# Kernel optimization log

Hardware: AMD Instinct MI355X
Metric: run time of the kernel (lower is better)

Reference implementation:

```python
import jax, jax.numpy as jnp
import numpy as np
import math

B, L, D, H = 4, 2048, 1024, 16
DK = D // H


def setup_inputs() -> dict:
    key = jax.random.key(0)
    ks = jax.random.split(key, 12)
    scale = math.sqrt(6.0 / (D + D))  # xavier_uniform for square Linear
    def lin(k):
        return jax.random.uniform(k, (D, D), jnp.float32, -scale, scale)
    inp = {
        "query": jax.random.normal(ks[0], (B, L, D), jnp.float32),
        "key": jax.random.normal(ks[1], (B, L, D), jnp.float32),
        "value": jax.random.normal(ks[2], (B, L, D), jnp.float32),
        "Wq": lin(ks[3]), "bq": jnp.zeros((D,), jnp.float32),
        "Wk": lin(ks[4]), "bk": jnp.zeros((D,), jnp.float32),
        "Wv": lin(ks[5]), "bv": jnp.zeros((D,), jnp.float32),
        "Wo": lin(ks[6]), "bo": jnp.zeros((D,), jnp.float32),
        # causal mask: True means masked (hide future positions)
        "attn_mask": jnp.triu(jnp.ones((L, L), dtype=bool), k=1),
    }
    return inp


def reference(query, key, value, Wq, bq, Wk, bk, Wv, bv, Wo, bo, attn_mask):
    def proj(x, W, b):
        # torch Linear: x @ W.T + b ; then split heads -> [B, H, L, DK]
        y = jnp.einsum('bld,ed->ble', x, W) + b
        return y.reshape(B, L, H, DK).transpose(0, 2, 1, 3)

    q = proj(query, Wq, bq)
    k = proj(key, Wk, bk)
    v = proj(value, Wv, bv)

    scores = jnp.einsum('bhqd,bhkd->bhqk', q, k) / jnp.sqrt(jnp.float32(DK))
    scores = jnp.where(attn_mask[None, None, :, :], jnp.float32(-jnp.inf), scores)
    p_attn = jax.nn.softmax(scores, axis=-1)  # dropout p=0 (eval)

    ctx = jnp.einsum('bhqk,bhkd->bhqd', p_attn, v)
    ctx = ctx.transpose(0, 2, 1, 3).reshape(B, L, D)
    out = jnp.einsum('bld,ed->ble', ctx, Wo) + bo
    return out
```

## Files before the change

### kernel.cpp

```cpp
#include <hip/hip_runtime.h>
#include <hip/hip_bf16.h>
#include <stdint.h>

typedef unsigned short u16;
typedef unsigned int u32;
typedef short short8 __attribute__((ext_vector_type(8)));
typedef float f32x4 __attribute__((ext_vector_type(4)));
typedef u32 u32x4 __attribute__((ext_vector_type(4)));
typedef u32 u32x2 __attribute__((ext_vector_type(2)));

#define DEV static __device__ __forceinline__

constexpr int Bsz = 4, Lseq = 2048, Dm = 1024, Hn = 16, Dk = 64;
constexpr float LOG2E = 1.44269504088896340736f;
constexpr float QSCALE = 0.125f * LOG2E;

DEV u16 f2bf(float x) {
    u32 u = __builtin_bit_cast(u32, x);
    return (u16)((u + 0x7fffu + ((u >> 16) & 1u)) >> 16);
}

DEV u32 pk2(float a, float b) {
    __hip_bfloat162 h = __float22bfloat162_rn(float2{a, b});
    u32 r;
    __builtin_memcpy(&r, &h, 4);
    return r;
}

DEV u32x4 ld8_cvt(const float* p) {
    f32x4 lo = *(const f32x4*)p;
    f32x4 hi = *(const f32x4*)(p + 4);
    u32x4 r;
    r[0] = pk2(lo[0], lo[1]);
    r[1] = pk2(lo[2], lo[3]);
    r[2] = pk2(hi[0], hi[1]);
    r[3] = pk2(hi[2], hi[3]);
    return r;
}

DEV void glds16(const void* g, void* l) {
    __builtin_amdgcn_global_load_lds(
        (const __attribute__((address_space(1))) void*)g,
        (__attribute__((address_space(3))) void*)l, 16, 0, 0);
}

__global__ __launch_bounds__(256) void cvt_f2b(
    const float* __restrict__ s, u16* __restrict__ d, int n8)
{
    int i = blockIdx.x * 256 + threadIdx.x;
    if (i >= n8) return;
    ((u32x4*)d)[i] = ld8_cvt(s + (long)i * 8);
}

template <int MODE>
__global__ __launch_bounds__(256) void gemm_glds(
    const u16* __restrict__ A, const u16* __restrict__ Bw,
    const float* __restrict__ bias, void* __restrict__ Cout, float scale)
{
    __shared__ u16 At[2][128 * 32];
    __shared__ u16 Bt[2][128 * 32];

    const int tid = threadIdx.x;
    const int lane = tid & 63, wid = tid >> 6;
    const int wr = wid >> 1, wc = wid & 1;
    const int mbase = blockIdx.x * 128, nbase = blockIdx.y * 128;

    f32x4 acc[4][4];
#pragma unroll
    for (int i = 0; i < 4; i++)
#pragma unroll
        for (int j = 0; j < 4; j++) acc[i][j] = (f32x4)0.f;

    const int srow = lane >> 2;
    const int sseg = (lane & 3) * 8;

    auto stage = [&](int kt, int buf) {
#pragma unroll
        for (int c = 0; c < 2; c++) {
            const int sec = wid * 2 + c;
            const long ko = (long)kt * 32 + sseg;
            glds16(A + (long)(mbase + sec * 16 + srow) * Dm + ko, &At[buf][sec * 512]);
            glds16(Bw + (long)(nbase + sec * 16 + srow) * Dm + ko, &Bt[buf][sec * 512]);
        }
    };

    stage(0, 0);
    __syncthreads();

    for (int kt = 0; kt < 32; kt++) {
        const int cur = kt & 1;
        if (kt + 1 < 32) stage(kt + 1, cur ^ 1);
        short8 af[4], bfr[4];
#pragma unroll
        for (int mf = 0; mf < 4; mf++)
            af[mf] = *(const short8*)&At[cur][(wr * 64 + mf * 16 + (lane & 15)) * 32 + (lane >> 4) * 8];
#pragma unroll
        for (int nf = 0; nf < 4; nf++)
            bfr[nf] = *(const short8*)&Bt[cur][(wc * 64 + nf * 16 + (lane & 15)) * 32 + (lane >> 4) * 8];
        __builtin_amdgcn_s_setprio(1);
#pragma unroll
        for (int mf = 0; mf < 4; mf++)
#pragma unroll
            for (int nf = 0; nf < 4; nf++)
                acc[mf][nf] = __builtin_amdgcn_mfma_f32_16x16x32_bf16(af[mf], bfr[nf], acc[mf][nf], 0, 0, 0);
        __builtin_amdgcn_s_setprio(0);
        __syncthreads();
    }

#pragma unroll
    for (int nf = 0; nf < 4; nf++) {
        const int n = nbase + wc * 64 + nf * 16 + (lane & 15);
        const float bv = bias[n];
#pragma unroll
        for (int mf = 0; mf < 4; mf++) {
            const int m0 = mbase + wr * 64 + mf * 16 + (lane >> 4) * 4;
#pragma unroll
            for (int r = 0; r < 4; r++) {
                const int m = m0 + r;
                const float v = (acc[mf][nf][r] + bv) * scale;
                if (MODE == 0) {
                    int b = m >> 11, l = m & 2047, h = n >> 6, dk = n & 63;
                    long addr = ((long)(b * Hn + h) * Lseq + l) * Dk + dk;
                    ((u16*)Cout)[addr] = f2bf(v);
                } else {
                    ((float*)Cout)[(long)m * Dm + n] = v;
                }
            }
        }
    }
}

__global__ __launch_bounds__(256) void gemm_hyb(
    const float* __restrict__ X, const u16* __restrict__ Bw,
    const float* __restrict__ bias, u16* __restrict__ Cout, float scale)
{
    __shared__ u16 At[2][128 * 32];
    __shared__ u16 Bt[2][128 * 32];

    const int tid = threadIdx.x;
    const int lane = tid & 63, wid = tid >> 6;
    const int wr = wid >> 1, wc = wid & 1;
    const int mbase = blockIdx.x * 128, nbase = blockIdx.y * 128;

    f32x4 acc[4][4];
#pragma unroll
    for (int i = 0; i < 4; i++)
#pragma unroll
        for (int j = 0; j < 4; j++) acc[i][j] = (f32x4)0.f;

    const int srow = lane >> 2;
    const int sseg = (lane & 3) * 8;
    auto stageB = [&](int kt, int buf) {
#pragma unroll
        for (int c = 0; c < 2; c++) {
            const int sec = wid * 2 + c;
            glds16(Bw + (long)(nbase + sec * 16 + srow) * Dm + (long)kt * 32 + sseg,
                   &Bt[buf][sec * 512]);
        }
    };

    u32x4 va[2];
    auto loadA = [&](int kt) {
#pragma unroll
        for (int i = 0; i < 2; i++) {
            int idx = i * 256 + tid;
            int row = idx >> 2, seg = idx & 3;
            va[i] = ld8_cvt(X + (long)(mbase + row) * Dm + (long)kt * 32 + seg * 8);
        }
    };
    auto writeA = [&](int buf) {
#pragma unroll
        for (int i = 0; i < 2; i++) {
            int idx = i * 256 + tid;
            *(u32x4*)&At[buf][idx * 8] = va[i];
        }
    };

    stageB(0, 0);
    loadA(0);
    writeA(0);
    __syncthreads();

    for (int kt = 0; kt < 32; kt++) {
        const int cur = kt & 1;
        const bool more = (kt + 1 < 32);
        if (more) {
            stageB(kt + 1, cur ^ 1);
            loadA(kt + 1);
        }
        short8 af[4], bfr[4];
#pragma unroll
        for (int mf = 0; mf < 4; mf++)
            af[mf] = *(const short8*)&At[cur][(wr * 64 + mf * 16 + (lane & 15)) * 32 + (lane >> 4) * 8];
#pragma unroll
        for (int nf = 0; nf < 4; nf++)
            bfr[nf] = *(const short8*)&Bt[cur][(wc * 64 + nf * 16 + (lane & 15)) * 32 + (lane >> 4) * 8];
        __builtin_amdgcn_s_setprio(1);
#pragma unroll
        for (int mf = 0; mf < 4; mf++)
#pragma unroll
            for (int nf = 0; nf < 4; nf++)
                acc[mf][nf] = __builtin_amdgcn_mfma_f32_16x16x32_bf16(af[mf], bfr[nf], acc[mf][nf], 0, 0, 0);
        __builtin_amdgcn_s_setprio(0);
        if (more) writeA(cur ^ 1);
        __syncthreads();
    }

#pragma unroll
    for (int nf = 0; nf < 4; nf++) {
        const int n = nbase + wc * 64 + nf * 16 + (lane & 15);
        const float bv = bias[n];
#pragma unroll
        for (int mf = 0; mf < 4; mf++) {
            const int m0 = mbase + wr * 64 + mf * 16 + (lane >> 4) * 4;
#pragma unroll
            for (int r = 0; r < 4; r++) {
                const int m = m0 + r;
                const float v = (acc[mf][nf][r] + bv) * scale;
                int b = m >> 11, l = m & 2047, h = n >> 6, dk = n & 63;
                long addr = ((long)(b * Hn + h) * Lseq + l) * Dk + dk;
                Cout[addr] = f2bf(v);
            }
        }
    }
}

__global__ __launch_bounds__(256) void attn_fwd(
    const u16* __restrict__ Qb, const u16* __restrict__ Kb,
    const u16* __restrict__ Vb, u16* __restrict__ Ctx)
{
    __shared__ u16 Kt[2][64 * 64];
    __shared__ u16 Vt[2][64 * 64];
    __shared__ u16 Pq[4][32 * 64];

    const int tid = threadIdx.x, lane = tid & 63, w = tid >> 6;
    const int qt = gridDim.y - 1 - blockIdx.y;
    const int bh = blockIdx.x;
    const long base = (long)bh * Lseq * Dk;
    const int qw = qt * 128 + w * 32;

    const int krow_in_w = lane >> 3;
    const int kseg = lane & 7;
    const int skv = tid >> 3, sdb = (tid & 7) * 8;

    auto stage_k = [&](int kvbase, int buf) {
#pragma unroll
        for (int c = 0; c < 2; c++) {
            int kv = w * 16 + c * 8 + krow_in_w;
            int d0 = ((kseg ^ (kv & 7)) * 8);
            glds16(Kb + base + (long)(kvbase + kv) * Dk + d0,
                   &Kt[buf][(w * 16 + c * 8) * 64]);
        }
    };

    short8 qfr[2][2];
#pragma unroll
    for (int qf = 0; qf < 2; qf++)
#pragma unroll
        for (int ks = 0; ks < 2; ks++) {
            int q = qw + qf * 16 + (lane & 15);
            int d0 = ks * 32 + (lane >> 4) * 8;
            qfr[qf][ks] = *(const short8*)(Qb + base + (long)q * Dk + d0);
        }

    f32x4 accT[4][2];
#pragma unroll
    for (int i = 0; i < 4; i++)
#pragma unroll
        for (int j = 0; j < 2; j++) accT[i][j] = (f32x4)0.f;
    float m_run[2] = {-__builtin_inff(), -__builtin_inff()};
    float l_part[2] = {0.f, 0.f};

    u32x4 vr[2];
    stage_k(0, 0);
#pragma unroll
    for (int i = 0; i < 2; i++)
        vr[i] = *(const u32x4*)(Vb + base + (long)(i * 32 + skv) * Dk + sdb);
#pragma unroll
    for (int i = 0; i < 2; i++) {
        int kv = i * 32 + skv;
        const u16* pv = (const u16*)&vr[i];
#pragma unroll
        for (int j = 0; j < 8; j++) {
            int d = sdb + j;
            Vt[0][d * 64 + (kv ^ ((((d & 7) ^ (d >> 3)) & 7) << 3))] = pv[j];
        }
    }
    __syncthreads();

    const int nkv = qt * 2 + 2;
    const int myn = ((qw + 31) >> 6) + 1;

    for (int kvt = 0; kvt < nkv; kvt++) {
        const int cur = kvt & 1;
        const bool more = (kvt + 1 < nkv);
        const int kvbase = kvt * 64;

        if (more) {
            stage_k(kvbase + 64, cur ^ 1);
#pragma unroll
            for (int i = 0; i < 2; i++)
                vr[i] = *(const u32x4*)(Vb + base + (long)(kvbase + 64 + i * 32 + skv) * Dk + sdb);
        }

        if (kvt < myn) {
            f32x4 st[4][2];
#pragma unroll
            for (int i = 0; i < 4; i++)
#pragma unroll
                for (int j = 0; j < 2; j++) st[i][j] = (f32x4)0.f;
            __builtin_amdgcn_s_setprio(1);
#pragma unroll
            for (int ks = 0; ks < 2; ks++) {
                short8 kf[4];
#pragma unroll
                for (int kvf = 0; kvf < 4; kvf++) {
                    int row = kvf * 16 + (lane & 15);
                    int d0 = ks * 32 + (lane >> 4) * 8;
                    kf[kvf] = *(const short8*)&Kt[cur][row * 64 + (d0 ^ ((row & 7) << 3))];
                }
#pragma unroll
                for (int kvf = 0; kvf < 4; kvf++)
#pragma unroll
                    for (int qf = 0; qf < 2; qf++)
                        st[kvf][qf] = __builtin_amdgcn_mfma_f32_16x16x32_bf16(kf[kvf], qfr[qf][ks], st[kvf][qf], 0, 0, 0);
            }
            __builtin_amdgcn_s_setprio(0);

            if ((kvbase + 63) > qw) {
#pragma unroll
                for (int qf = 0; qf < 2; qf++) {
                    const int q = qw + qf * 16 + (lane & 15);
#pragma unroll
                    for (int kvf = 0; kvf < 4; kvf++)
#pragma unroll
                        for (int r = 0; r < 4; r++) {
                            int kv = kvbase + kvf * 16 + (lane >> 4) * 4 + r;
                            if (kv > q) st[kvf][qf][r] = -1e30f;
                        }
                }
            }

#pragma unroll
            for (int qf = 0; qf < 2; qf++) {
                float tmax = st[0][qf][0];
#pragma unroll
                for (int kvf = 0; kvf < 4; kvf++)
#pragma unroll
                    for (int r = 0; r < 4; r++) tmax = fmaxf(tmax, st[kvf][qf][r]);
                tmax = fmaxf(tmax, __shfl_xor(tmax, 16, 64));
                tmax = fmaxf(tmax, __shfl_xor(tmax, 32, 64));
                const bool norescale = __all((int)(tmax <= m_run[qf] + 8.f));
                if (!norescale) {
                    const float mnew = fmaxf(m_run[qf], tmax);
                    const float sc = __builtin_exp2f(m_run[qf] - mnew);
                    m_run[qf] = mnew;
                    l_part[qf] *= sc;
#pragma unroll
                    for (int dkf = 0; dkf < 4; dkf++)
#pragma unroll
                        for (int r = 0; r < 4; r++) accT[dkf][qf][r] *= sc;
                }
                const float mq = m_run[qf];
                float ts = 0.f;
#pragma unroll
                for (int kvf = 0; kvf < 4; kvf++)
#pragma unroll
                    for (int r = 0; r < 4; r++) {
                        float p = __builtin_exp2f(st[kvf][qf][r] - mq);
                        st[kvf][qf][r] = p;
                        ts += p;
                    }
                l_part[qf] += ts;
                const int qrow = qf * 16 + (lane & 15);
#pragma unroll
                for (int kvf = 0; kvf < 4; kvf++) {
                    u32x2 pk;
                    pk[0] = pk2(st[kvf][qf][0], st[kvf][qf][1]);
                    pk[1] = pk2(st[kvf][qf][2], st[kvf][qf][3]);
                    int kvi = (kvf * 16 + (lane >> 4) * 4) ^ ((lane & 7) << 3);
                    *(u32x2*)&Pq[w][qrow * 64 + kvi] = pk;
                }
            }

#pragma unroll
            for (int kf2 = 0; kf2 < 2; kf2++) {
                short8 vfr[4];
#pragma unroll
                for (int dkf = 0; dkf < 4; dkf++) {
                    int d = dkf * 16 + (lane & 15);
                    int kvi = (kf2 * 32 + (lane >> 4) * 8) ^ ((((d & 7) ^ (d >> 3)) & 7) << 3);
                    vfr[dkf] = *(const short8*)&Vt[cur][d * 64 + kvi];
                }
                short8 pfr[2];
#pragma unroll
                for (int qf = 0; qf < 2; qf++) {
                    int qrow = qf * 16 + (lane & 15);
                    int kvi = (kf2 * 32 + (lane >> 4) * 8) ^ ((lane & 7) << 3);
                    pfr[qf] = *(const short8*)&Pq[w][qrow * 64 + kvi];
                }
                __builtin_amdgcn_s_setprio(1);
#pragma unroll
                for (int dkf = 0; dkf < 4; dkf++)
#pragma unroll
                    for (int qf = 0; qf < 2; qf++)
                        accT[dkf][qf] = __builtin_amdgcn_mfma_f32_16x16x32_bf16(vfr[dkf], pfr[qf], accT[dkf][qf], 0, 0, 0);
                __builtin_amdgcn_s_setprio(0);
            }
        }

        if (more) {
#pragma unroll
            for (int i = 0; i < 2; i++) {
                int kv = i * 32 + skv;
                const u16* pv = (const u16*)&vr[i];
#pragma unroll
                for (int j = 0; j < 8; j++) {
                    int d = sdb + j;
                    Vt[cur ^ 1][d * 64 + (kv ^ ((((d & 7) ^ (d >> 3)) & 7) << 3))] = pv[j];
                }
            }
        }
        __syncthreads();
    }

    const int b = bh >> 4, h = bh & 15;
#pragma unroll
    for (int qf = 0; qf < 2; qf++) {
        float l = l_part[qf];
        l += __shfl_xor(l, 16, 64);
        l += __shfl_xor(l, 32, 64);
        const float inv = 1.f / l;
        const int q = qw + qf * 16 + (lane & 15);
#pragma unroll
        for (int dkf = 0; dkf < 4; dkf++) {
            const int dk0 = dkf * 16 + (lane >> 4) * 4;
            u32x2 o;
            o[0] = pk2(accT[dkf][qf][0] * inv, accT[dkf][qf][1] * inv);
            o[1] = pk2(accT[dkf][qf][2] * inv, accT[dkf][qf][3] * inv);
            long addr = ((long)b * Lseq + q) * Dm + h * Dk + dk0;
            *(u32x2*)(Ctx + addr) = o;
        }
    }
}

extern "C" void kernel_launch(void* const* d_in, const int* in_sizes, int n_in,
                              void* d_out, int out_size, void* d_ws, size_t ws_size,
                              hipStream_t stream)
{
    const float* query = (const float*)d_in[0];
    const float* key_  = (const float*)d_in[1];
    const float* value = (const float*)d_in[2];
    const float* Wq = (const float*)d_in[3];
    const float* bq = (const float*)d_in[4];
    const float* Wk = (const float*)d_in[5];
    const float* bk = (const float*)d_in[6];
    const float* Wv = (const float*)d_in[7];
    const float* bv = (const float*)d_in[8];
    const float* Wo = (const float*)d_in[9];
    const float* bo = (const float*)d_in[10];

    float* out = (float*)d_out;
    const size_t tens = (size_t)Bsz * Lseq * Dm;
    const size_t wTot = (size_t)Dm * Dm;
    u16* Qb = (u16*)d_ws;
    u16* Kb = Qb + tens;
    u16* Vb = Kb + tens;
    u16* Cx = Vb + tens;
    u16* Wqb = Cx;
    u16* Wkb = Wqb + wTot;
    u16* Wvb = Wkb + wTot;
    u16* Wob = Qb;

    dim3 blk(256), g(64, 8);
    const int n8w = (int)(wTot / 8);
    const int gw = (n8w + 255) / 256;

    cvt_f2b<<<gw, blk, 0, stream>>>(Wq, Wqb, n8w);
    cvt_f2b<<<gw, blk, 0, stream>>>(Wk, Wkb, n8w);
    cvt_f2b<<<gw, blk, 0, stream>>>(Wv, Wvb, n8w);
    gemm_hyb<<<g, blk, 0, stream>>>(query, Wqb, bq, Qb, QSCALE);
    gemm_hyb<<<g, blk, 0, stream>>>(key_,  Wkb, bk, Kb, 1.0f);
    gemm_hyb<<<g, blk, 0, stream>>>(value, Wvb, bv, Vb, 1.0f);
    attn_fwd<<<dim3(Bsz * Hn, Lseq / 128), blk, 0, stream>>>(Qb, Kb, Vb, Cx);
    cvt_f2b<<<gw, blk, 0, stream>>>(Wo, Wob, n8w);
    gemm_glds<1><<<g, blk, 0, stream>>>(Cx, Wob, bo, out, 1.0f);
}
```

Measured before the change: 243.6 us.

## Batch Q/K/V projections into one launch and shrink attention P scratch

Folds the three separate Q, K and V projection GEMM launches into a single kernel with a 3x larger grid. Each block picks its input, weight slice, bias and output by blockIdx.y, which fills the GPU better and removes two launches. In the attention kernel the P tile is now written to LDS per 32-wide kv half right before its PV MFMA, halving the Pq shared buffer. That lowers LDS use and could allow more resident blocks, at the cost of two 8-byte reads per fragment instead of one 16-byte read, plus a new swizzle pattern that must stay correct.

```diff
diff --git a/kernel.cpp b/kernel.cpp
--- a/kernel.cpp
+++ b/kernel.cpp
@@ -52,10 +52,9 @@
     ((u32x4*)d)[i] = ld8_cvt(s + (long)i * 8);
 }
 
-template <int MODE>
 __global__ __launch_bounds__(256) void gemm_glds(
     const u16* __restrict__ A, const u16* __restrict__ Bw,
-    const float* __restrict__ bias, void* __restrict__ Cout, float scale)
+    const float* __restrict__ bias, float* __restrict__ Cout, float scale)
 {
     __shared__ u16 At[2][128 * 32];
     __shared__ u16 Bt[2][128 * 32];
@@ -117,22 +116,17 @@
 #pragma unroll
             for (int r = 0; r < 4; r++) {
                 const int m = m0 + r;
-                const float v = (acc[mf][nf][r] + bv) * scale;
-                if (MODE == 0) {
-                    int b = m >> 11, l = m & 2047, h = n >> 6, dk = n & 63;
-                    long addr = ((long)(b * Hn + h) * Lseq + l) * Dk + dk;
-                    ((u16*)Cout)[addr] = f2bf(v);
-                } else {
-                    ((float*)Cout)[(long)m * Dm + n] = v;
-                }
-            }
-        }
-    }
-}
-
-__global__ __launch_bounds__(256) void gemm_hyb(
-    const float* __restrict__ X, const u16* __restrict__ Bw,
-    const float* __restrict__ bias, u16* __restrict__ Cout, float scale)
+                Cout[(long)m * Dm + n] = (acc[mf][nf][r] + bv) * scale;
+            }
+        }
+    }
+}
+
+__global__ __launch_bounds__(256) void gemm_qkv(
+    const float* __restrict__ Xq, const float* __restrict__ Xk,
+    const float* __restrict__ Xv, const u16* __restrict__ Wb3,
+    const float* __restrict__ bq, const float* __restrict__ bk,
+    const float* __restrict__ bv, u16* __restrict__ Out3)
 {
     __shared__ u16 At[2][128 * 32];
     __shared__ u16 Bt[2][128 * 32];
@@ -140,7 +134,14 @@
     const int tid = threadIdx.x;
     const int lane = tid & 63, wid = tid >> 6;
     const int wr = wid >> 1, wc = wid & 1;
-    const int mbase = blockIdx.x * 128, nbase = blockIdx.y * 128;
+    const int mbase = blockIdx.x * 128;
+    const int t = blockIdx.y >> 3;
+    const int nbase = (blockIdx.y & 7) * 128;
+    const float* X = t == 0 ? Xq : (t == 1 ? Xk : Xv);
+    const u16* Bw = Wb3 + (size_t)t * Dm * Dm;
+    const float* bias = t == 0 ? bq : (t == 1 ? bk : bv);
+    const float scale = t == 0 ? QSCALE : 1.0f;
+    u16* Cout = Out3 + (size_t)t * ((size_t)Bsz * Lseq * Dm);
 
     f32x4 acc[4][4];
 #pragma unroll
@@ -231,7 +232,7 @@
 {
     __shared__ u16 Kt[2][64 * 64];
     __shared__ u16 Vt[2][64 * 64];
-    __shared__ u16 Pq[4][32 * 64];
+    __shared__ u16 Pq[4][32 * 32];
 
     const int tid = threadIdx.x, lane = tid & 63, w = tid >> 6;
     const int qt = gridDim.y - 1 - blockIdx.y;
@@ -372,19 +373,23 @@
                         ts += p;
                     }
                 l_part[qf] += ts;
-                const int qrow = qf * 16 + (lane & 15);
-#pragma unroll
-                for (int kvf = 0; kvf < 4; kvf++) {
-                    u32x2 pk;
-                    pk[0] = pk2(st[kvf][qf][0], st[kvf][qf][1]);
-                    pk[1] = pk2(st[kvf][qf][2], st[kvf][qf][3]);
-                    int kvi = (kvf * 16 + (lane >> 4) * 4) ^ ((lane & 7) << 3);
-                    *(u32x2*)&Pq[w][qrow * 64 + kvi] = pk;
-                }
             }
 
 #pragma unroll
             for (int kf2 = 0; kf2 < 2; kf2++) {
+#pragma unroll
+                for (int qf = 0; qf < 2; qf++) {
+                    const int qrow = qf * 16 + (lane & 15);
+#pragma unroll
+                    for (int k2 = 0; k2 < 2; k2++) {
+                        const int kvf = kf2 * 2 + k2;
+                        u32x2 pk;
+                        pk[0] = pk2(st[kvf][qf][0], st[kvf][qf][1]);
+                        pk[1] = pk2(st[kvf][qf][2], st[kvf][qf][3]);
+                        const int kvi = (k2 * 16 + (lane >> 4) * 4) ^ ((lane & 7) << 2);
+                        *(u32x2*)&Pq[w][qrow * 32 + kvi] = pk;
+                    }
+                }
                 short8 vfr[4];
 #pragma unroll
                 for (int dkf = 0; dkf < 4; dkf++) {
@@ -395,9 +400,14 @@
                 short8 pfr[2];
 #pragma unroll
                 for (int qf = 0; qf < 2; qf++) {
-                    int qrow = qf * 16 + (lane & 15);
-                    int kvi = (kf2 * 32 + (lane >> 4) * 8) ^ ((lane & 7) << 3);
-                    pfr[qf] = *(const short8*)&Pq[w][qrow * 64 + kvi];
+                    const int qrow = qf * 16 + (lane & 15);
+                    u32x2 lohi[2];
+#pragma unroll
+                    for (int h = 0; h < 2; h++) {
+                        const int kvi = ((lane >> 4) * 8 + h * 4) ^ ((lane & 7) << 2);
+                        lohi[h] = *(const u32x2*)&Pq[w][qrow * 32 + kvi];
+                    }
+                    __builtin_memcpy(&pfr[qf], lohi, 16);
                 }
                 __builtin_amdgcn_s_setprio(1);
 #pragma unroll
@@ -472,17 +482,15 @@
     u16* Wvb = Wkb + wTot;
     u16* Wob = Qb;
 
-    dim3 blk(256), g(64, 8);
+    dim3 blk(256), g(64, 8), gq(64, 24);
     const int n8w = (int)(wTot / 8);
     const int gw = (n8w + 255) / 256;
 
     cvt_f2b<<<gw, blk, 0, stream>>>(Wq, Wqb, n8w);
     cvt_f2b<<<gw, blk, 0, stream>>>(Wk, Wkb, n8w);
     cvt_f2b<<<gw, blk, 0, stream>>>(Wv, Wvb, n8w);
-    gemm_hyb<<<g, blk, 0, stream>>>(query, Wqb, bq, Qb, QSCALE);
-    gemm_hyb<<<g, blk, 0, stream>>>(key_,  Wkb, bk, Kb, 1.0f);
-    gemm_hyb<<<g, blk, 0, stream>>>(value, Wvb, bv, Vb, 1.0f);
+    gemm_qkv<<<gq, blk, 0, stream>>>(query, key_, value, Wqb, bq, bk, bv, Qb);
     attn_fwd<<<dim3(Bsz * Hn, Lseq / 128), blk, 0, stream>>>(Qb, Kb, Vb, Cx);
     cvt_f2b<<<gw, blk, 0, stream>>>(Wo, Wob, n8w);
-    gemm_glds<1><<<g, blk, 0, stream>>>(Cx, Wob, bo, out, 1.0f);
-}
+    gemm_glds<<<g, blk, 0, stream>>>(Cx, Wob, bo, out, 1.0f);
+}
```

Result: faster. 223.8 us (-8.2%).
